# Kernel optimization log

Hardware: AMD Instinct MI355X
Metric: run time of the kernel (lower is better)

## Reference

```python
import jax, jax.numpy as jnp
import numpy as np
from jax import lax

N = 64            # n_channels
L = 5             # n_layers
CLS = 12          # n_classes
B = 262144        # batch
NUM_MZI = N * (N - 1) // 2
C_HALF = 0.7071067811865476  # sqrt(0.5)
RESP = 0.8        # photodiode_responsivity
SENS = 0.001      # sensitivity
GAMMA = 0.05      # fwhm / 2

# MZI pair indices in the same order as the torch double loop (i, then j>i)
_II, _JJ = np.triu_indices(N, k=1)
_II = jnp.asarray(_II, dtype=jnp.int32)
_JJ = jnp.asarray(_JJ, dtype=jnp.int32)


def construct_unitary(mzi_phases, output_phases):
    # mzi_phases: [NUM_MZI*2] interleaved (theta, phi); output_phases: [N]
    thetas = mzi_phases[0::2]
    phis = mzi_phases[1::2]

    def step(U, inp):
        i, j, theta, phi = inp
        ui = U[i]
        uj = U[j]
        e_phi = jnp.exp(1j * phi)
        e_theta = jnp.exp(1j * theta)
        new_i = C_HALF * ui + C_HALF * e_phi * uj
        new_j = C_HALF * e_theta * ui - C_HALF * e_theta * e_phi * uj
        U = U.at[i].set(new_i).at[j].set(new_j)
        return U, None

    U0 = jnp.eye(N, dtype=jnp.complex64)
    U, _ = lax.scan(step, U0, (_II, _JJ, thetas, phis))
    # output phase screen: diag(exp(i*phase)) @ U
    return jnp.exp(1j * output_phases)[:, None] * U


def nofu(field, beta_param, initial_detuning):
    beta = jax.nn.sigmoid(beta_param)                       # [N]
    input_power = jnp.abs(field) ** 2                       # [B, N]
    detuning = initial_detuning + SENS * RESP * beta * input_power
    transmission = GAMMA / (GAMMA + 1j * detuning)          # complex Lorentzian
    return jnp.sqrt(jax.nn.relu(1.0 - beta)) * field * transmission


def setup_inputs() -> dict:
    key = jax.random.key(0)
    ks = jax.random.split(key, 12)
    return {
        "x": jax.random.normal(ks[0], (B, N), dtype=jnp.float32),
        "mzi_phases": 0.1 * jax.random.normal(ks[1], (L, NUM_MZI * 2), dtype=jnp.float32),
        "output_phases": 0.1 * jax.random.normal(ks[2], (L, N), dtype=jnp.float32),
        "beta_param": 0.1 * jax.random.normal(ks[3], (L - 1, N), dtype=jnp.float32),
        "initial_detuning": 0.1 * jax.random.normal(ks[4], (L - 1, N), dtype=jnp.float32),
        "W1": 0.1 * jax.random.normal(ks[5], (2 * N, N), dtype=jnp.float32),
        "b1": jnp.zeros((2 * N,), dtype=jnp.float32),
        "W2": 0.1 * jax.random.normal(ks[6], (N, 2 * N), dtype=jnp.float32),
        "b2": jnp.zeros((N,), dtype=jnp.float32),
        "W3": 0.1 * jax.random.normal(ks[7], (CLS, N), dtype=jnp.float32),
        "b3": jnp.zeros((CLS,), dtype=jnp.float32),
    }


def reference(x, mzi_phases, output_phases, beta_param, initial_detuning,
              W1, b1, W2, b2, W3, b3):
    field = x.astype(jnp.complex64)                         # [B, N]
    for l in range(L):
        U = construct_unitary(mzi_phases[l], output_phases[l])  # [N, N] complex
        field = jnp.einsum("ij,bj->bi", U, field)
        if l < L - 1:
            field = nofu(field, beta_param[l], initial_detuning[l])
    power = jnp.abs(field) ** 2                             # [B, N] real
    h = jax.nn.relu(power @ W1.T + b1)
    h = jax.nn.relu(h @ W2.T + b2)
    return h @ W3.T + b3                                    # [B, CLS]
```

## Files before the change

kernel.cpp:

```cpp
#include <hip/hip_runtime.h>
#include <math.h>


#define NN 64
#define LL 5
#define NMZI 2016
#define C_HALF 0.7071067811865476f
#define GAMMA_ 0.05f
#define SENSRESP 0.0008f

#define AH_SHORTS   114688
#define FLOAT_BYTE  458752

typedef short short8 __attribute__((ext_vector_type(8)));
typedef float f32x4  __attribute__((ext_vector_type(4)));

__device__ __forceinline__ unsigned short f2bf(float f) {
    unsigned u = __float_as_uint(f);
    unsigned r = u + 0x7fffu + ((u >> 16) & 1u);
    return (unsigned short)(r >> 16);
}
__device__ __forceinline__ float bf2f(unsigned short h) {
    return __uint_as_float(((unsigned)h) << 16);
}
__device__ __forceinline__ unsigned packsplit(float v) {
    unsigned short h = f2bf(v);
    float lo = v - bf2f(h);
    return (unsigned)h | (((unsigned)f2bf(lo)) << 16);
}
__device__ __forceinline__ int afrag_off(int l, int m, int k) {
    return ((((l * 8 + (m >> 4)) * 4 + (k >> 5)) << 9)
          + ((((k >> 3) & 3) * 16 + (m & 15)) << 3) + (k & 7));
}

__global__ __launch_bounds__(64) void build_unitaries(
    const float* __restrict__ mzi, const float* __restrict__ oph,
    unsigned short* __restrict__ AH)
{
    unsigned short* AL = AH + AH_SHORTS;
    const int l = blockIdx.x;
    const int c = threadIdx.x;

    __shared__ float cs[NMZI][4];
    __shared__ float ocs[NN][2];

    for (int m = c; m < NMZI; m += 64) {
        float th = mzi[l * 2 * NMZI + 2 * m];
        float ph = mzi[l * 2 * NMZI + 2 * m + 1];
        float sth, cth, sph, cph;
        sincosf(th, &sth, &cth);
        sincosf(ph, &sph, &cph);
        cs[m][0] = cph; cs[m][1] = sph;
        cs[m][2] = C_HALF * cth; cs[m][3] = C_HALF * sth;
    }
    {
        float ps = oph[l * NN + c];
        float sp, cp; sincosf(ps, &sp, &cp);
        ocs[c][0] = cp; ocs[c][1] = sp;
    }
    __syncthreads();

    float ur[NN], ui[NN];
    #pragma unroll
    for (int r = 0; r < NN; ++r) { ur[r] = (r == c) ? 1.f : 0.f; ui[r] = 0.f; }

    int m = 0;
    #pragma unroll
    for (int i = 0; i < NN - 1; ++i) {
        #pragma unroll
        for (int j = i + 1; j < NN; ++j) {
            float cph = cs[m][0], sph = cs[m][1];
            float cct = cs[m][2], cst = cs[m][3];
            float tr = cph * ur[j] - sph * ui[j];
            float ti = cph * ui[j] + sph * ur[j];
            float ar = ur[i] + tr, ai = ui[i] + ti;
            float sr = ur[i] - tr, si = ui[i] - ti;
            ur[i] = C_HALF * ar;
            ui[i] = C_HALF * ai;
            ur[j] = cct * sr - cst * si;
            ui[j] = cct * si + cst * sr;
            ++m;
        }
    }
    #pragma unroll
    for (int r = 0; r < NN; ++r) {
        float cp = ocs[r][0], sp = ocs[r][1];
        float vr = cp * ur[r] - sp * ui[r];
        float vi = cp * ui[r] + sp * ur[r];
        ur[r] = vr; ui[r] = vi;
    }
    #pragma unroll
    for (int mm = 0; mm < 128; ++mm) {
        float v1 = (mm < 64) ? ur[mm] : ui[mm - 64];
        float v2 = (mm < 64) ? -ui[mm] : ur[mm - 64];
        int o1 = afrag_off(l, mm, c);
        int o2 = afrag_off(l, mm, c + 64);
        unsigned short h1 = f2bf(v1), h2 = f2bf(v2);
        AH[o1] = h1; AL[o1] = f2bf(v1 - bf2f(h1));
        AH[o2] = h2; AL[o2] = f2bf(v2 - bf2f(h2));
    }
}

__global__ void prep_weights(const float* __restrict__ W1,
                             const float* __restrict__ W2,
                             const float* __restrict__ W3,
                             const float* __restrict__ beta_param,
                             const float* __restrict__ det0,
                             unsigned short* __restrict__ AH)
{
    unsigned short* AL = AH + AH_SHORTS;
    float* fbase = (float*)((char*)AH + FLOAT_BYTE);
    float* nofuF = fbase;
    float* W3T   = fbase + 1024;

    int idx = blockIdx.x * 256 + threadIdx.x;
    if (idx < 8192) {
        int mm = idx >> 6, k = idx & 63;
        float v = W1[idx];
        unsigned short h = f2bf(v);
        int o = afrag_off(5, mm, k);
        AH[o] = h; AL[o] = f2bf(v - bf2f(h));
    } else if (idx < 16384) {
        int t = idx - 8192;
        int mm = t >> 7, k = t & 127;
        float v = W2[t];
        unsigned short h = f2bf(v);
        int o = afrag_off(6, mm, k);
        AH[o] = h; AL[o] = f2bf(v - bf2f(h));
    } else if (idx < 17152) {
        int t = idx - 16384;
        int r = t >> 6, j = t & 63;
        W3T[j * 12 + r] = W3[t];
    } else if (idx < 17408) {
        int t = idx - 17152;
        float bp = beta_param[t];
        float beta = 1.f / (1.f + expf(-bp));
        float* p = nofuF + t * 4;
        p[0] = SENSRESP * beta;
        p[1] = sqrtf(fmaxf(1.f - beta, 0.f)) * GAMMA_;
        p[2] = det0[t];
        p[3] = 0.f;
    }
}

#define FS 132

__global__ __launch_bounds__(256, 2) void ficonn_main(
    const float* __restrict__ x,
    const float* __restrict__ b1,
    const float* __restrict__ b2,
    const float* __restrict__ b3,
    const unsigned short* __restrict__ AH,
    const float4* __restrict__ nofuC,
    const float* __restrict__ W3T,
    float* __restrict__ out)
{
    const unsigned short* AL = AH + AH_SHORTS;
    __shared__ __align__(16) unsigned F[128 * FS];

    const int tid  = threadIdx.x;
    const int lane = tid & 63;
    const int w    = tid >> 6;
    const int mp   = w & 1, nh = w >> 1;
    const int n16  = lane & 15, q = lane >> 4;
    const int base = blockIdx.x * 128;

    {
        const float4* x4 = (const float4*)(x + (size_t)base * 64);
        #pragma unroll
        for (int it = 0; it < 8; ++it) {
            int idx = tid + it * 256;
            int j4 = idx & 15, ss = idx >> 4;
            float4 v = x4[idx];
            uint4 pk = make_uint4(packsplit(v.x), packsplit(v.y),
                                  packsplit(v.z), packsplit(v.w));
            *(uint4*)&F[ss * FS + 4 * j4] = pk;
        }
    }
    __syncthreads();

    f32x4 acc[4][4];

    for (int l = 0; l < 5; ++l) {
        #pragma unroll
        for (int i = 0; i < 4; ++i)
            #pragma unroll
            for (int t = 0; t < 4; ++t)
                #pragma unroll
                for (int r = 0; r < 4; ++r) acc[i][t][r] = 0.f;

        const int K4 = (l == 0) ? 2 : 4;
        for (int Kt = 0; Kt < K4; ++Kt) {
            uint4 ahu[4], alu[4];
            #pragma unroll
            for (int i = 0; i < 4; ++i) {
                int Mt = 2 * mp + (i & 1) + 4 * (i >> 1);
                int off = (((l * 8 + Mt) * 4 + Kt) << 9);
                ahu[i] = ((const uint4*)(AH + off))[lane];
                alu[i] = ((const uint4*)(AL + off))[lane];
            }
            uint4 bq0[4], bq1[4];
            #pragma unroll
            for (int t = 0; t < 4; ++t) {
                int n = 64 * nh + 16 * t + n16;
                const uint4* p = (const uint4*)&F[n * FS + 32 * Kt + 8 * q];
                bq0[t] = p[0]; bq1[t] = p[1];
            }
            #pragma unroll
            for (int t = 0; t < 4; ++t) {
                union { short8 s; unsigned u[4]; } bh, bl;
                unsigned uu[8] = {bq0[t].x, bq0[t].y, bq0[t].z, bq0[t].w,
                                  bq1[t].x, bq1[t].y, bq1[t].z, bq1[t].w};
                #pragma unroll
                for (int e = 0; e < 4; ++e) {
                    unsigned a = uu[2 * e], b = uu[2 * e + 1];
                    bh.u[e] = (a & 0xffffu) | (b << 16);
                    bl.u[e] = (a >> 16) | (b & 0xffff0000u);
                }
                #pragma unroll
                for (int i = 0; i < 4; ++i) {
                    union { short8 s; uint4 u4; } ah_, al_;
                    ah_.u4 = ahu[i]; al_.u4 = alu[i];
                    acc[i][t] = __builtin_amdgcn_mfma_f32_16x16x32_bf16(ah_.s, bh.s, acc[i][t], 0, 0, 0);
                    acc[i][t] = __builtin_amdgcn_mfma_f32_16x16x32_bf16(ah_.s, bl.s, acc[i][t], 0, 0, 0);
                    acc[i][t] = __builtin_amdgcn_mfma_f32_16x16x32_bf16(al_.s, bh.s, acc[i][t], 0, 0, 0);
                }
            }
        }
        __syncthreads();

        if (l < 4) {
            #pragma unroll
            for (int i = 0; i < 2; ++i) {
                int Mt = 2 * mp + i;
                float4 nc[4];
                #pragma unroll
                for (int r = 0; r < 4; ++r)
                    nc[r] = nofuC[l * 64 + 16 * Mt + 4 * q + r];
                #pragma unroll
                for (int t = 0; t < 4; ++t) {
                    int n = 64 * nh + 16 * t + n16;
                    unsigned wr[4], wi[4];
                    #pragma unroll
                    for (int r = 0; r < 4; ++r) {
                        float yr = acc[i][t][r], yi = acc[i + 2][t][r];
                        float4 c = nc[r];
                        float p   = fmaf(yr, yr, yi * yi);
                        float det = fmaf(c.x, p, c.z);
                        float sc  = c.y * __builtin_amdgcn_rcpf(fmaf(det, det, GAMMA_ * GAMMA_));
                        wr[r] = packsplit(sc * fmaf( det, yi, GAMMA_ * yr));
                        wi[r] = packsplit(sc * fmaf(-det, yr, GAMMA_ * yi));
                    }
                    int k0 = 16 * Mt + 4 * q;
                    *(uint4*)&F[n * FS + k0]      = make_uint4(wr[0], wr[1], wr[2], wr[3]);
                    *(uint4*)&F[n * FS + 64 + k0] = make_uint4(wi[0], wi[1], wi[2], wi[3]);
                }
            }
        } else {
            #pragma unroll
            for (int i = 0; i < 2; ++i) {
                int Mt = 2 * mp + i;
                #pragma unroll
                for (int t = 0; t < 4; ++t) {
                    int n = 64 * nh + 16 * t + n16;
                    unsigned wp[4];
                    #pragma unroll
                    for (int r = 0; r < 4; ++r) {
                        float yr = acc[i][t][r], yi = acc[i + 2][t][r];
                        wp[r] = packsplit(fmaf(yr, yr, yi * yi));
                    }
                    *(uint4*)&F[n * FS + 16 * Mt + 4 * q] = make_uint4(wp[0], wp[1], wp[2], wp[3]);
                }
            }
        }
        __syncthreads();
    }

    {
        #pragma unroll
        for (int i = 0; i < 4; ++i)
            #pragma unroll
            for (int t = 0; t < 4; ++t)
                #pragma unroll
                for (int r = 0; r < 4; ++r) acc[i][t][r] = 0.f;

        for (int Kt = 0; Kt < 2; ++Kt) {
            uint4 ahu[4], alu[4];
            #pragma unroll
            for (int i = 0; i < 4; ++i) {
                int Mt = 4 * mp + i;
                int off = (((5 * 8 + Mt) * 4 + Kt) << 9);
                ahu[i] = ((const uint4*)(AH + off))[lane];
                alu[i] = ((const uint4*)(AL + off))[lane];
            }
            uint4 bq0[4], bq1[4];
            #pragma unroll
            for (int t = 0; t < 4; ++t) {
                int n = 64 * nh + 16 * t + n16;
                const uint4* p = (const uint4*)&F[n * FS + 32 * Kt + 8 * q];
                bq0[t] = p[0]; bq1[t] = p[1];
            }
            #pragma unroll
            for (int t = 0; t < 4; ++t) {
                union { short8 s; unsigned u[4]; } bh, bl;
                unsigned uu[8] = {bq0[t].x, bq0[t].y, bq0[t].z, bq0[t].w,
                                  bq1[t].x, bq1[t].y, bq1[t].z, bq1[t].w};
                #pragma unroll
                for (int e = 0; e < 4; ++e) {
                    unsigned a = uu[2 * e], b = uu[2 * e + 1];
                    bh.u[e] = (a & 0xffffu) | (b << 16);
                    bl.u[e] = (a >> 16) | (b & 0xffff0000u);
                }
                #pragma unroll
                for (int i = 0; i < 4; ++i) {
                    union { short8 s; uint4 u4; } ah_, al_;
                    ah_.u4 = ahu[i]; al_.u4 = alu[i];
                    acc[i][t] = __builtin_amdgcn_mfma_f32_16x16x32_bf16(ah_.s, bh.s, acc[i][t], 0, 0, 0);
                    acc[i][t] = __builtin_amdgcn_mfma_f32_16x16x32_bf16(ah_.s, bl.s, acc[i][t], 0, 0, 0);
                    acc[i][t] = __builtin_amdgcn_mfma_f32_16x16x32_bf16(al_.s, bh.s, acc[i][t], 0, 0, 0);
                }
            }
        }
        __syncthreads();

        #pragma unroll
        for (int i = 0; i < 4; ++i) {
            int Mt = 4 * mp + i;
            float4 bb = *(const float4*)&b1[16 * Mt + 4 * q];
            #pragma unroll
            for (int t = 0; t < 4; ++t) {
                int n = 64 * nh + 16 * t + n16;
                unsigned wv[4];
                #pragma unroll
                for (int r = 0; r < 4; ++r) {
                    float h = fmaxf(acc[i][t][r] + ((const float*)&bb)[r], 0.f);
                    wv[r] = packsplit(h);
                }
                *(uint4*)&F[n * FS + 16 * Mt + 4 * q] = make_uint4(wv[0], wv[1], wv[2], wv[3]);
            }
        }
        __syncthreads();
    }

    {
        #pragma unroll
        for (int i = 0; i < 2; ++i)
            #pragma unroll
            for (int t = 0; t < 4; ++t)
                #pragma unroll
                for (int r = 0; r < 4; ++r) acc[i][t][r] = 0.f;

        for (int Kt = 0; Kt < 4; ++Kt) {
            uint4 ahu[2], alu[2];
            #pragma unroll
            for (int i = 0; i < 2; ++i) {
                int Mt = 2 * mp + i;
                int off = (((6 * 8 + Mt) * 4 + Kt) << 9);
                ahu[i] = ((const uint4*)(AH + off))[lane];
                alu[i] = ((const uint4*)(AL + off))[lane];
            }
            uint4 bq0[4], bq1[4];
            #pragma unroll
            for (int t = 0; t < 4; ++t) {
                int n = 64 * nh + 16 * t + n16;
                const uint4* p = (const uint4*)&F[n * FS + 32 * Kt + 8 * q];
                bq0[t] = p[0]; bq1[t] = p[1];
            }
            #pragma unroll
            for (int t = 0; t < 4; ++t) {
                union { short8 s; unsigned u[4]; } bh, bl;
                unsigned uu[8] = {bq0[t].x, bq0[t].y, bq0[t].z, bq0[t].w,
                                  bq1[t].x, bq1[t].y, bq1[t].z, bq1[t].w};
                #pragma unroll
                for (int e = 0; e < 4; ++e) {
                    unsigned a = uu[2 * e], b = uu[2 * e + 1];
                    bh.u[e] = (a & 0xffffu) | (b << 16);
                    bl.u[e] = (a >> 16) | (b & 0xffff0000u);
                }
                #pragma unroll
                for (int i = 0; i < 2; ++i) {
                    union { short8 s; uint4 u4; } ah_, al_;
                    ah_.u4 = ahu[i]; al_.u4 = alu[i];
                    acc[i][t] = __builtin_amdgcn_mfma_f32_16x16x32_bf16(ah_.s, bh.s, acc[i][t], 0, 0, 0);
                    acc[i][t] = __builtin_amdgcn_mfma_f32_16x16x32_bf16(ah_.s, bl.s, acc[i][t], 0, 0, 0);
                    acc[i][t] = __builtin_amdgcn_mfma_f32_16x16x32_bf16(al_.s, bh.s, acc[i][t], 0, 0, 0);
                }
            }
        }
        __syncthreads();

        #pragma unroll
        for (int i = 0; i < 2; ++i) {
            int Mt = 2 * mp + i;
            float4 bb = *(const float4*)&b2[16 * Mt + 4 * q];
            #pragma unroll
            for (int t = 0; t < 4; ++t) {
                int n = 64 * nh + 16 * t + n16;
                unsigned wv[4];
                #pragma unroll
                for (int r = 0; r < 4; ++r) {
                    float h = fmaxf(acc[i][t][r] + ((const float*)&bb)[r], 0.f);
                    wv[r] = packsplit(h);
                }
                *(uint4*)&F[n * FS + 16 * Mt + 4 * q] = make_uint4(wv[0], wv[1], wv[2], wv[3]);
            }
        }
        __syncthreads();
    }

    if (tid < 128) {
        int n = tid;
        float o[12];
        #pragma unroll
        for (int r = 0; r < 12; ++r) o[r] = b3[r];
        #pragma unroll
        for (int kc = 0; kc < 16; ++kc) {
            uint4 pk = *(const uint4*)&F[n * FS + 4 * kc];
            unsigned uu[4] = {pk.x, pk.y, pk.z, pk.w};
            #pragma unroll
            for (int e = 0; e < 4; ++e) {
                int k = 4 * kc + e;
                float h = bf2f((unsigned short)(uu[e] & 0xffffu))
                        + bf2f((unsigned short)(uu[e] >> 16));
                const float* wr = W3T + k * 12;
                #pragma unroll
                for (int r = 0; r < 12; ++r) o[r] = fmaf(wr[r], h, o[r]);
            }
        }
        float4* op = (float4*)(out + (size_t)(base + n) * 12);
        op[0] = make_float4(o[0], o[1], o[2],  o[3]);
        op[1] = make_float4(o[4], o[5], o[6],  o[7]);
        op[2] = make_float4(o[8], o[9], o[10], o[11]);
    }
}

extern "C" void kernel_launch(void* const* d_in, const int* in_sizes, int n_in,
                              void* d_out, int out_size, void* d_ws, size_t ws_size,
                              hipStream_t stream)
{
    const float* x    = (const float*)d_in[0];
    const float* mzi  = (const float*)d_in[1];
    const float* oph  = (const float*)d_in[2];
    const float* beta = (const float*)d_in[3];
    const float* det0 = (const float*)d_in[4];
    const float* W1   = (const float*)d_in[5];
    const float* b1   = (const float*)d_in[6];
    const float* W2   = (const float*)d_in[7];
    const float* b2   = (const float*)d_in[8];
    const float* W3   = (const float*)d_in[9];
    const float* b3   = (const float*)d_in[10];
    float* out = (float*)d_out;

    unsigned short* AH = (unsigned short*)d_ws;
    float* fbase = (float*)((char*)d_ws + FLOAT_BYTE);
    const float4* nofuC = (const float4*)fbase;
    const float* W3T = fbase + 1024;

    const int B = in_sizes[0] / NN;
    const int blocks = B / 128;

    hipLaunchKernelGGL(build_unitaries, dim3(LL), dim3(64), 0, stream, mzi, oph, AH);
    hipLaunchKernelGGL(prep_weights, dim3(68), dim3(256), 0, stream,
                       W1, W2, W3, beta, det0, AH);
    hipLaunchKernelGGL(ficonn_main, dim3(blocks), dim3(256), 0, stream,
                       x, b1, b2, b3, AH, nofuC, W3T, out);
}
```

Before: 376.5 us.

## Split hi/lo bf16 planes in LDS, use 512-thread blocks, prefetch MZI coefficients

The main kernel now stores activations as separate hi and lo bf16 planes in dynamic LDS, so MFMA B-operands load directly as short8 without per-element repacking. The block grows to 8 waves, each owning one M-tile pair (real and imaginary), which halves per-wave accumulators and is meant to raise occupancy. The hi/lo split now uses byte permutes, and the matmul code is folded into a templated helper. The unitary builder uses 256 threads for the sincos setup and keeps a rolling 16-entry register prefetch of MZI coefficients, which adds register pressure.

```diff
diff --git a/kernel.cpp b/kernel.cpp
--- a/kernel.cpp
+++ b/kernel.cpp
@@ -11,9 +11,14 @@
 
 #define AH_SHORTS   114688
 #define FLOAT_BYTE  458752
+#define FROW 136
 
 typedef short short8 __attribute__((ext_vector_type(8)));
 typedef float f32x4  __attribute__((ext_vector_type(4)));
+
+union U4S8 { uint4 u; short8 s; };
+
+#define MFMA16(a, b, c) __builtin_amdgcn_mfma_f32_16x16x32_bf16((a), (b), (c), 0, 0, 0)
 
 __device__ __forceinline__ unsigned short f2bf(float f) {
     unsigned u = __float_as_uint(f);
@@ -23,70 +28,88 @@
 __device__ __forceinline__ float bf2f(unsigned short h) {
     return __uint_as_float(((unsigned)h) << 16);
 }
-__device__ __forceinline__ unsigned packsplit(float v) {
-    unsigned short h = f2bf(v);
-    float lo = v - bf2f(h);
-    return (unsigned)h | (((unsigned)f2bf(lo)) << 16);
+__device__ __forceinline__ unsigned rnebits(float v) {
+    unsigned u = __float_as_uint(v);
+    return u + 0x7fffu + ((u >> 16) & 1u);
+}
+__device__ __forceinline__ unsigned permhi16(unsigned a, unsigned b) {
+    return __builtin_amdgcn_perm(a, b, 0x03020706);
+}
+__device__ __forceinline__ void split4(const float* v, uint2& hi, uint2& lo) {
+    unsigned r0 = rnebits(v[0]), r1 = rnebits(v[1]);
+    unsigned r2 = rnebits(v[2]), r3 = rnebits(v[3]);
+    hi.x = permhi16(r0, r1);
+    hi.y = permhi16(r2, r3);
+    float l0 = v[0] - __uint_as_float(r0 & 0xffff0000u);
+    float l1 = v[1] - __uint_as_float(r1 & 0xffff0000u);
+    float l2 = v[2] - __uint_as_float(r2 & 0xffff0000u);
+    float l3 = v[3] - __uint_as_float(r3 & 0xffff0000u);
+    lo.x = permhi16(__float_as_uint(l0), __float_as_uint(l1));
+    lo.y = permhi16(__float_as_uint(l2), __float_as_uint(l3));
 }
 __device__ __forceinline__ int afrag_off(int l, int m, int k) {
     return ((((l * 8 + (m >> 4)) * 4 + (k >> 5)) << 9)
           + ((((k >> 3) & 3) * 16 + (m & 15)) << 3) + (k & 7));
 }
 
-__global__ __launch_bounds__(64) void build_unitaries(
+__global__ __launch_bounds__(256, 1) void build_unitaries(
     const float* __restrict__ mzi, const float* __restrict__ oph,
     unsigned short* __restrict__ AH)
 {
     unsigned short* AL = AH + AH_SHORTS;
     const int l = blockIdx.x;
-    const int c = threadIdx.x;
-
-    __shared__ float cs[NMZI][4];
-    __shared__ float ocs[NN][2];
-
-    for (int m = c; m < NMZI; m += 64) {
+    const int tid = threadIdx.x;
+
+    __shared__ float4 cs4[NMZI];
+    __shared__ float2 ocs2[NN];
+
+    for (int m = tid; m < NMZI; m += 256) {
         float th = mzi[l * 2 * NMZI + 2 * m];
         float ph = mzi[l * 2 * NMZI + 2 * m + 1];
         float sth, cth, sph, cph;
         sincosf(th, &sth, &cth);
         sincosf(ph, &sph, &cph);
-        cs[m][0] = cph; cs[m][1] = sph;
-        cs[m][2] = C_HALF * cth; cs[m][3] = C_HALF * sth;
-    }
-    {
-        float ps = oph[l * NN + c];
-        float sp, cp; sincosf(ps, &sp, &cp);
-        ocs[c][0] = cp; ocs[c][1] = sp;
+        cs4[m] = make_float4(cph, sph, C_HALF * cth, C_HALF * sth);
+    }
+    if (tid < NN) {
+        float sp, cp; sincosf(oph[l * NN + tid], &sp, &cp);
+        ocs2[tid] = make_float2(cp, sp);
     }
     __syncthreads();
+    if (tid >= 64) return;
+    const int c = tid;
 
     float ur[NN], ui[NN];
     #pragma unroll
     for (int r = 0; r < NN; ++r) { ur[r] = (r == c) ? 1.f : 0.f; ui[r] = 0.f; }
 
+    float4 qb[16];
+    #pragma unroll
+    for (int t = 0; t < 16; ++t) qb[t] = cs4[t];
+
     int m = 0;
     #pragma unroll
     for (int i = 0; i < NN - 1; ++i) {
         #pragma unroll
         for (int j = i + 1; j < NN; ++j) {
-            float cph = cs[m][0], sph = cs[m][1];
-            float cct = cs[m][2], cst = cs[m][3];
-            float tr = cph * ur[j] - sph * ui[j];
-            float ti = cph * ui[j] + sph * ur[j];
+            float4 qq = qb[m & 15];
+            if (m + 16 < NMZI) qb[m & 15] = cs4[m + 16];
+            float tr = qq.x * ur[j] - qq.y * ui[j];
+            float ti = qq.x * ui[j] + qq.y * ur[j];
             float ar = ur[i] + tr, ai = ui[i] + ti;
             float sr = ur[i] - tr, si = ui[i] - ti;
             ur[i] = C_HALF * ar;
             ui[i] = C_HALF * ai;
-            ur[j] = cct * sr - cst * si;
-            ui[j] = cct * si + cst * sr;
+            ur[j] = qq.z * sr - qq.w * si;
+            ui[j] = qq.z * si + qq.w * sr;
             ++m;
         }
     }
     #pragma unroll
     for (int r = 0; r < NN; ++r) {
-        float cp = ocs[r][0], sp = ocs[r][1];
-        float vr = cp * ur[r] - sp * ui[r];
-        float vi = cp * ui[r] + sp * ur[r];
+        float2 oc = ocs2[r];
+        float vr = oc.x * ur[r] - oc.y * ui[r];
+        float vi = oc.x * ui[r] + oc.y * ur[r];
         ur[r] = vr; ui[r] = vi;
     }
     #pragma unroll
@@ -143,9 +166,40 @@
     }
 }
 
-#define FS 132
-
-__global__ __launch_bounds__(256, 2) void ficonn_main(
+template<int K4, bool PAIR>
+__device__ __forceinline__ void mm_block(
+    const unsigned short* __restrict__ AH, const unsigned short* __restrict__ AL,
+    const unsigned short* Fh, const unsigned short* Fl,
+    int slot, int mt0, int lane, int q, const int* brow,
+    f32x4* acc0, f32x4* acc1)
+{
+    #pragma unroll
+    for (int Kt = 0; Kt < K4; ++Kt) {
+        int off0 = (((slot * 8 + mt0) * 4 + Kt) << 9);
+        U4S8 ah0, al0, ah1, al1;
+        ah0.u = ((const uint4*)(AH + off0))[lane];
+        al0.u = ((const uint4*)(AL + off0))[lane];
+        if (PAIR) {
+            ah1.u = ((const uint4*)(AH + off0 + 8192))[lane];
+            al1.u = ((const uint4*)(AL + off0 + 8192))[lane];
+        }
+        #pragma unroll
+        for (int t = 0; t < 4; ++t) {
+            short8 bh = *(const short8*)&Fh[brow[t] + 32 * Kt + 8 * q];
+            short8 bl = *(const short8*)&Fl[brow[t] + 32 * Kt + 8 * q];
+            acc0[t] = MFMA16(ah0.s, bh, acc0[t]);
+            acc0[t] = MFMA16(ah0.s, bl, acc0[t]);
+            acc0[t] = MFMA16(al0.s, bh, acc0[t]);
+            if (PAIR) {
+                acc1[t] = MFMA16(ah1.s, bh, acc1[t]);
+                acc1[t] = MFMA16(ah1.s, bl, acc1[t]);
+                acc1[t] = MFMA16(al1.s, bh, acc1[t]);
+            }
+        }
+    }
+}
+
+__global__ __launch_bounds__(512, 4) void ficonn_main(
     const float* __restrict__ x,
     const float* __restrict__ b1,
     const float* __restrict__ b2,
@@ -156,254 +210,143 @@
     float* __restrict__ out)
 {
     const unsigned short* AL = AH + AH_SHORTS;
-    __shared__ __align__(16) unsigned F[128 * FS];
+    extern __shared__ unsigned short Fdyn[];
+    unsigned short* Fh = Fdyn;
+    unsigned short* Fl = Fdyn + 128 * FROW;
 
     const int tid  = threadIdx.x;
     const int lane = tid & 63;
-    const int w    = tid >> 6;
-    const int mp   = w & 1, nh = w >> 1;
+    const int w    = __builtin_amdgcn_readfirstlane(tid >> 6);
+    const int mp   = w & 3, nh = w >> 2;
     const int n16  = lane & 15, q = lane >> 4;
     const int base = blockIdx.x * 128;
 
     {
         const float4* x4 = (const float4*)(x + (size_t)base * 64);
         #pragma unroll
-        for (int it = 0; it < 8; ++it) {
-            int idx = tid + it * 256;
+        for (int it = 0; it < 4; ++it) {
+            int idx = tid + it * 512;
             int j4 = idx & 15, ss = idx >> 4;
-            float4 v = x4[idx];
-            uint4 pk = make_uint4(packsplit(v.x), packsplit(v.y),
-                                  packsplit(v.z), packsplit(v.w));
-            *(uint4*)&F[ss * FS + 4 * j4] = pk;
+            float4 v4 = x4[idx];
+            float vv[4] = {v4.x, v4.y, v4.z, v4.w};
+            uint2 hi, lo; split4(vv, hi, lo);
+            *(uint2*)&Fh[ss * FROW + 4 * j4] = hi;
+            *(uint2*)&Fl[ss * FROW + 4 * j4] = lo;
         }
     }
     __syncthreads();
 
-    f32x4 acc[4][4];
-
+    int brow[4];
+    #pragma unroll
+    for (int t = 0; t < 4; ++t) brow[t] = (64 * nh + 16 * t + n16) * FROW;
+    const int kw = 16 * mp + 4 * q;
+
+    #pragma unroll 1
     for (int l = 0; l < 5; ++l) {
-        #pragma unroll
-        for (int i = 0; i < 4; ++i)
-            #pragma unroll
-            for (int t = 0; t < 4; ++t)
+        f32x4 acc0[4], acc1[4];
+        #pragma unroll
+        for (int t = 0; t < 4; ++t)
+            #pragma unroll
+            for (int r = 0; r < 4; ++r) { acc0[t][r] = 0.f; acc1[t][r] = 0.f; }
+
+        if (l == 0) mm_block<2, true>(AH, AL, Fh, Fl, 0, mp, lane, q, brow, acc0, acc1);
+        else        mm_block<4, true>(AH, AL, Fh, Fl, l, mp, lane, q, brow, acc0, acc1);
+        __syncthreads();
+
+        if (l < 4) {
+            float4 nc[4];
+            #pragma unroll
+            for (int r = 0; r < 4; ++r) nc[r] = nofuC[l * 64 + kw + r];
+            #pragma unroll
+            for (int t = 0; t < 4; ++t) {
+                float wr[4], wi[4];
                 #pragma unroll
-                for (int r = 0; r < 4; ++r) acc[i][t][r] = 0.f;
-
-        const int K4 = (l == 0) ? 2 : 4;
-        for (int Kt = 0; Kt < K4; ++Kt) {
-            uint4 ahu[4], alu[4];
-            #pragma unroll
-            for (int i = 0; i < 4; ++i) {
-                int Mt = 2 * mp + (i & 1) + 4 * (i >> 1);
-                int off = (((l * 8 + Mt) * 4 + Kt) << 9);
-                ahu[i] = ((const uint4*)(AH + off))[lane];
-                alu[i] = ((const uint4*)(AL + off))[lane];
+                for (int r = 0; r < 4; ++r) {
+                    float yr = acc0[t][r], yi = acc1[t][r];
+                    float4 c = nc[r];
+                    float p   = fmaf(yr, yr, yi * yi);
+                    float det = fmaf(c.x, p, c.z);
+                    float sc  = c.y * __builtin_amdgcn_rcpf(fmaf(det, det, GAMMA_ * GAMMA_));
+                    float tr = sc * GAMMA_, ti = sc * det;
+                    wr[r] = fmaf(tr, yr,  ti * yi);
+                    wi[r] = fmaf(tr, yi, -ti * yr);
+                }
+                uint2 hi, lo;
+                split4(wr, hi, lo);
+                *(uint2*)&Fh[brow[t] + kw] = hi;
+                *(uint2*)&Fl[brow[t] + kw] = lo;
+                split4(wi, hi, lo);
+                *(uint2*)&Fh[brow[t] + kw + 64] = hi;
+                *(uint2*)&Fl[brow[t] + kw + 64] = lo;
             }
-            uint4 bq0[4], bq1[4];
+        } else {
             #pragma unroll
             for (int t = 0; t < 4; ++t) {
-                int n = 64 * nh + 16 * t + n16;
-                const uint4* p = (const uint4*)&F[n * FS + 32 * Kt + 8 * q];
-                bq0[t] = p[0]; bq1[t] = p[1];
-            }
-            #pragma unroll
-            for (int t = 0; t < 4; ++t) {
-                union { short8 s; unsigned u[4]; } bh, bl;
-                unsigned uu[8] = {bq0[t].x, bq0[t].y, bq0[t].z, bq0[t].w,
-                                  bq1[t].x, bq1[t].y, bq1[t].z, bq1[t].w};
-                #pragma unroll
-                for (int e = 0; e < 4; ++e) {
-                    unsigned a = uu[2 * e], b = uu[2 * e + 1];
-                    bh.u[e] = (a & 0xffffu) | (b << 16);
-                    bl.u[e] = (a >> 16) | (b & 0xffff0000u);
-                }
-                #pragma unroll
-                for (int i = 0; i < 4; ++i) {
-                    union { short8 s; uint4 u4; } ah_, al_;
-                    ah_.u4 = ahu[i]; al_.u4 = alu[i];
-                    acc[i][t] = __builtin_amdgcn_mfma_f32_16x16x32_bf16(ah_.s, bh.s, acc[i][t], 0, 0, 0);
-                    acc[i][t] = __builtin_amdgcn_mfma_f32_16x16x32_bf16(ah_.s, bl.s, acc[i][t], 0, 0, 0);
-                    acc[i][t] = __builtin_amdgcn_mfma_f32_16x16x32_bf16(al_.s, bh.s, acc[i][t], 0, 0, 0);
-                }
-            }
-        }
-        __syncthreads();
-
-        if (l < 4) {
-            #pragma unroll
-            for (int i = 0; i < 2; ++i) {
-                int Mt = 2 * mp + i;
-                float4 nc[4];
+                float pw[4];
                 #pragma unroll
                 for (int r = 0; r < 4; ++r)
-                    nc[r] = nofuC[l * 64 + 16 * Mt + 4 * q + r];
-                #pragma unroll
-                for (int t = 0; t < 4; ++t) {
-                    int n = 64 * nh + 16 * t + n16;
-                    unsigned wr[4], wi[4];
-                    #pragma unroll
-                    for (int r = 0; r < 4; ++r) {
-                        float yr = acc[i][t][r], yi = acc[i + 2][t][r];
-                        float4 c = nc[r];
-                        float p   = fmaf(yr, yr, yi * yi);
-                        float det = fmaf(c.x, p, c.z);
-                        float sc  = c.y * __builtin_amdgcn_rcpf(fmaf(det, det, GAMMA_ * GAMMA_));
-                        wr[r] = packsplit(sc * fmaf( det, yi, GAMMA_ * yr));
-                        wi[r] = packsplit(sc * fmaf(-det, yr, GAMMA_ * yi));
-                    }
-                    int k0 = 16 * Mt + 4 * q;
-                    *(uint4*)&F[n * FS + k0]      = make_uint4(wr[0], wr[1], wr[2], wr[3]);
-                    *(uint4*)&F[n * FS + 64 + k0] = make_uint4(wi[0], wi[1], wi[2], wi[3]);
-                }
+                    pw[r] = fmaf(acc0[t][r], acc0[t][r], acc1[t][r] * acc1[t][r]);
+                uint2 hi, lo;
+                split4(pw, hi, lo);
+                *(uint2*)&Fh[brow[t] + kw] = hi;
+                *(uint2*)&Fl[brow[t] + kw] = lo;
             }
-        } else {
-            #pragma unroll
-            for (int i = 0; i < 2; ++i) {
-                int Mt = 2 * mp + i;
-                #pragma unroll
-                for (int t = 0; t < 4; ++t) {
-                    int n = 64 * nh + 16 * t + n16;
-                    unsigned wp[4];
-                    #pragma unroll
-                    for (int r = 0; r < 4; ++r) {
-                        float yr = acc[i][t][r], yi = acc[i + 2][t][r];
-                        wp[r] = packsplit(fmaf(yr, yr, yi * yi));
-                    }
-                    *(uint4*)&F[n * FS + 16 * Mt + 4 * q] = make_uint4(wp[0], wp[1], wp[2], wp[3]);
-                }
+        }
+        __syncthreads();
+    }
+
+    {
+        f32x4 acc0[4], acc1[4];
+        #pragma unroll
+        for (int t = 0; t < 4; ++t)
+            #pragma unroll
+            for (int r = 0; r < 4; ++r) { acc0[t][r] = 0.f; acc1[t][r] = 0.f; }
+
+        mm_block<2, true>(AH, AL, Fh, Fl, 5, mp, lane, q, brow, acc0, acc1);
+        __syncthreads();
+
+        float4 bb0 = *(const float4*)&b1[kw];
+        float4 bb1 = *(const float4*)&b1[kw + 64];
+        #pragma unroll
+        for (int t = 0; t < 4; ++t) {
+            float h0[4], h1v[4];
+            #pragma unroll
+            for (int r = 0; r < 4; ++r) {
+                h0[r]  = fmaxf(acc0[t][r] + ((const float*)&bb0)[r], 0.f);
+                h1v[r] = fmaxf(acc1[t][r] + ((const float*)&bb1)[r], 0.f);
             }
+            uint2 hi, lo;
+            split4(h0, hi, lo);
+            *(uint2*)&Fh[brow[t] + kw] = hi;
+            *(uint2*)&Fl[brow[t] + kw] = lo;
+            split4(h1v, hi, lo);
+            *(uint2*)&Fh[brow[t] + kw + 64] = hi;
+            *(uint2*)&Fl[brow[t] + kw + 64] = lo;
         }
         __syncthreads();
     }
 
     {
-        #pragma unroll
-        for (int i = 0; i < 4; ++i)
-            #pragma unroll
-            for (int t = 0; t < 4; ++t)
-                #pragma unroll
-                for (int r = 0; r < 4; ++r) acc[i][t][r] = 0.f;
-
-        for (int Kt = 0; Kt < 2; ++Kt) {
-            uint4 ahu[4], alu[4];
-            #pragma unroll
-            for (int i = 0; i < 4; ++i) {
-                int Mt = 4 * mp + i;
-                int off = (((5 * 8 + Mt) * 4 + Kt) << 9);
-                ahu[i] = ((const uint4*)(AH + off))[lane];
-                alu[i] = ((const uint4*)(AL + off))[lane];
-            }
-            uint4 bq0[4], bq1[4];
-            #pragma unroll
-            for (int t = 0; t < 4; ++t) {
-                int n = 64 * nh + 16 * t + n16;
-                const uint4* p = (const uint4*)&F[n * FS + 32 * Kt + 8 * q];
-                bq0[t] = p[0]; bq1[t] = p[1];
-            }
-            #pragma unroll
-            for (int t = 0; t < 4; ++t) {
-                union { short8 s; unsigned u[4]; } bh, bl;
-                unsigned uu[8] = {bq0[t].x, bq0[t].y, bq0[t].z, bq0[t].w,
-                                  bq1[t].x, bq1[t].y, bq1[t].z, bq1[t].w};
-                #pragma unroll
-                for (int e = 0; e < 4; ++e) {
-                    unsigned a = uu[2 * e], b = uu[2 * e + 1];
-                    bh.u[e] = (a & 0xffffu) | (b << 16);
-                    bl.u[e] = (a >> 16) | (b & 0xffff0000u);
-                }
-                #pragma unroll
-                for (int i = 0; i < 4; ++i) {
-                    union { short8 s; uint4 u4; } ah_, al_;
-                    ah_.u4 = ahu[i]; al_.u4 = alu[i];
-                    acc[i][t] = __builtin_amdgcn_mfma_f32_16x16x32_bf16(ah_.s, bh.s, acc[i][t], 0, 0, 0);
-                    acc[i][t] = __builtin_amdgcn_mfma_f32_16x16x32_bf16(ah_.s, bl.s, acc[i][t], 0, 0, 0);
-                    acc[i][t] = __builtin_amdgcn_mfma_f32_16x16x32_bf16(al_.s, bh.s, acc[i][t], 0, 0, 0);
-                }
-            }
-        }
-        __syncthreads();
-
-        #pragma unroll
-        for (int i = 0; i < 4; ++i) {
-            int Mt = 4 * mp + i;
-            float4 bb = *(const float4*)&b1[16 * Mt + 4 * q];
-            #pragma unroll
-            for (int t = 0; t < 4; ++t) {
-                int n = 64 * nh + 16 * t + n16;
-                unsigned wv[4];
-                #pragma unroll
-                for (int r = 0; r < 4; ++r) {
-                    float h = fmaxf(acc[i][t][r] + ((const float*)&bb)[r], 0.f);
-                    wv[r] = packsplit(h);
-                }
-                *(uint4*)&F[n * FS + 16 * Mt + 4 * q] = make_uint4(wv[0], wv[1], wv[2], wv[3]);
-            }
-        }
-        __syncthreads();
-    }
-
-    {
-        #pragma unroll
-        for (int i = 0; i < 2; ++i)
-            #pragma unroll
-            for (int t = 0; t < 4; ++t)
-                #pragma unroll
-                for (int r = 0; r < 4; ++r) acc[i][t][r] = 0.f;
-
-        for (int Kt = 0; Kt < 4; ++Kt) {
-            uint4 ahu[2], alu[2];
-            #pragma unroll
-            for (int i = 0; i < 2; ++i) {
-                int Mt = 2 * mp + i;
-                int off = (((6 * 8 + Mt) * 4 + Kt) << 9);
-                ahu[i] = ((const uint4*)(AH + off))[lane];
-                alu[i] = ((const uint4*)(AL + off))[lane];
-            }
-            uint4 bq0[4], bq1[4];
-            #pragma unroll
-            for (int t = 0; t < 4; ++t) {
-                int n = 64 * nh + 16 * t + n16;
-                const uint4* p = (const uint4*)&F[n * FS + 32 * Kt + 8 * q];
-                bq0[t] = p[0]; bq1[t] = p[1];
-            }
-            #pragma unroll
-            for (int t = 0; t < 4; ++t) {
-                union { short8 s; unsigned u[4]; } bh, bl;
-                unsigned uu[8] = {bq0[t].x, bq0[t].y, bq0[t].z, bq0[t].w,
-                                  bq1[t].x, bq1[t].y, bq1[t].z, bq1[t].w};
-                #pragma unroll
-                for (int e = 0; e < 4; ++e) {
-                    unsigned a = uu[2 * e], b = uu[2 * e + 1];
-                    bh.u[e] = (a & 0xffffu) | (b << 16);
-                    bl.u[e] = (a >> 16) | (b & 0xffff0000u);
-                }
-                #pragma unroll
-                for (int i = 0; i < 2; ++i) {
-                    union { short8 s; uint4 u4; } ah_, al_;
-                    ah_.u4 = ahu[i]; al_.u4 = alu[i];
-                    acc[i][t] = __builtin_amdgcn_mfma_f32_16x16x32_bf16(ah_.s, bh.s, acc[i][t], 0, 0, 0);
-                    acc[i][t] = __builtin_amdgcn_mfma_f32_16x16x32_bf16(ah_.s, bl.s, acc[i][t], 0, 0, 0);
-                    acc[i][t] = __builtin_amdgcn_mfma_f32_16x16x32_bf16(al_.s, bh.s, acc[i][t], 0, 0, 0);
-                }
-            }
-        }
-        __syncthreads();
-
-        #pragma unroll
-        for (int i = 0; i < 2; ++i) {
-            int Mt = 2 * mp + i;
-            float4 bb = *(const float4*)&b2[16 * Mt + 4 * q];
-            #pragma unroll
-            for (int t = 0; t < 4; ++t) {
-                int n = 64 * nh + 16 * t + n16;
-                unsigned wv[4];
-                #pragma unroll
-                for (int r = 0; r < 4; ++r) {
-                    float h = fmaxf(acc[i][t][r] + ((const float*)&bb)[r], 0.f);
-                    wv[r] = packsplit(h);
-                }
-                *(uint4*)&F[n * FS + 16 * Mt + 4 * q] = make_uint4(wv[0], wv[1], wv[2], wv[3]);
-            }
+        f32x4 acc0[4], acc1[4];
+        #pragma unroll
+        for (int t = 0; t < 4; ++t)
+            #pragma unroll
+            for (int r = 0; r < 4; ++r) acc0[t][r] = 0.f;
+
+        mm_block<4, false>(AH, AL, Fh, Fl, 6, mp, lane, q, brow, acc0, acc1);
+        __syncthreads();
+
+        float4 bb = *(const float4*)&b2[kw];
+        #pragma unroll
+        for (int t = 0; t < 4; ++t) {
+            float h[4];
+            #pragma unroll
+            for (int r = 0; r < 4; ++r)
+                h[r] = fmaxf(acc0[t][r] + ((const float*)&bb)[r], 0.f);
+            uint2 hi, lo;
+            split4(h, hi, lo);
+            *(uint2*)&Fh[brow[t] + kw] = hi;
+            *(uint2*)&Fl[brow[t] + kw] = lo;
         }
         __syncthreads();
     }
@@ -413,18 +356,25 @@
         float o[12];
         #pragma unroll
         for (int r = 0; r < 12; ++r) o[r] = b3[r];
-        #pragma unroll
-        for (int kc = 0; kc < 16; ++kc) {
-            uint4 pk = *(const uint4*)&F[n * FS + 4 * kc];
-            unsigned uu[4] = {pk.x, pk.y, pk.z, pk.w};
+        const unsigned short* rh = &Fh[n * FROW];
+        const unsigned short* rl = &Fl[n * FROW];
+        #pragma unroll
+        for (int kc = 0; kc < 8; ++kc) {
+            uint4 ph = *(const uint4*)&rh[8 * kc];
+            uint4 pl = *(const uint4*)&rl[8 * kc];
+            unsigned hu[4] = {ph.x, ph.y, ph.z, ph.w};
+            unsigned lu[4] = {pl.x, pl.y, pl.z, pl.w};
             #pragma unroll
             for (int e = 0; e < 4; ++e) {
-                int k = 4 * kc + e;
-                float h = bf2f((unsigned short)(uu[e] & 0xffffu))
-                        + bf2f((unsigned short)(uu[e] >> 16));
-                const float* wr = W3T + k * 12;
+                int k = 8 * kc + 2 * e;
+                float ha = __uint_as_float(hu[e] << 16) + __uint_as_float(lu[e] << 16);
+                float hb = __uint_as_float(hu[e] & 0xffff0000u)
+                         + __uint_as_float(lu[e] & 0xffff0000u);
+                const float* wa = W3T + k * 12;
+                const float* wb = W3T + (k + 1) * 12;
                 #pragma unroll
-                for (int r = 0; r < 12; ++r) o[r] = fmaf(wr[r], h, o[r]);
+                for (int r = 0; r < 12; ++r)
+                    o[r] = fmaf(wa[r], ha, fmaf(wb[r], hb, o[r]));
             }
         }
         float4* op = (float4*)(out + (size_t)(base + n) * 12);
@@ -458,10 +408,11 @@
 
     const int B = in_sizes[0] / NN;
     const int blocks = B / 128;
-
-    hipLaunchKernelGGL(build_unitaries, dim3(LL), dim3(64), 0, stream, mzi, oph, AH);
+    const size_t lds_bytes = 2u * 128u * FROW * sizeof(unsigned short);
+
+    hipLaunchKernelGGL(build_unitaries, dim3(LL), dim3(256), 0, stream, mzi, oph, AH);
     hipLaunchKernelGGL(prep_weights, dim3(68), dim3(256), 0, stream,
                        W1, W2, W3, beta, det0, AH);
-    hipLaunchKernelGGL(ficonn_main, dim3(blocks), dim3(256), 0, stream,
+    hipLaunchKernelGGL(ficonn_main, dim3(blocks), dim3(512), lds_bytes, stream,
                        x, b1, b2, b3, AH, nofuC, W3T, out);
 }
```

Measured after the change: 708.0 us. 88.1% more time.
